# Kernel optimization log

Measured on AMD Instinct MI355X. Metric: run time of the kernel, lower is better.

## Reference

```python
import jax, jax.numpy as jnp
import numpy as np

N_NODES = 100000
N_EDGES = 1600000
IN_CH = 128
HID = 128
BN_EPS = 1e-5


def setup_inputs() -> dict:
    key = jax.random.key(0)
    ks = jax.random.split(key, 16)
    x = jax.random.normal(ks[0], (N_NODES, IN_CH), dtype=jnp.float32)
    edge_index = jax.random.randint(ks[1], (2, N_EDGES), 0, N_NODES, dtype=jnp.int32)
    edge_attr = jax.random.uniform(ks[2], (N_EDGES,), dtype=jnp.float32)
    def glorot(k, fan_in, fan_out):
        s = jnp.sqrt(6.0 / (fan_in + fan_out))
        return jax.random.uniform(k, (fan_in, fan_out), dtype=jnp.float32, minval=-s, maxval=s)
    W1 = glorot(ks[3], IN_CH, HID)
    b1 = jnp.zeros((HID,), jnp.float32)
    gamma1 = jnp.ones((HID,), jnp.float32)
    beta1 = jnp.zeros((HID,), jnp.float32)
    W2 = glorot(ks[4], HID, HID)
    b2 = jnp.zeros((HID,), jnp.float32)
    gamma2 = jnp.ones((HID,), jnp.float32)
    beta2 = jnp.zeros((HID,), jnp.float32)
    W3 = glorot(ks[5], HID, 1)
    b3 = jnp.zeros((1,), jnp.float32)
    return {"x": x, "edge_index": edge_index, "edge_attr": edge_attr,
            "W1": W1, "b1": b1, "gamma1": gamma1, "beta1": beta1,
            "W2": W2, "b2": b2, "gamma2": gamma2, "beta2": beta2,
            "W3": W3, "b3": b3}


def _gcn_norm(edge_index, edge_weight, num_nodes):
    # PyG gcn_norm with add_self_loops=True, self-loop weight 1.0
    sl = jnp.arange(num_nodes, dtype=edge_index.dtype)
    row = jnp.concatenate([edge_index[0], sl])  # source
    col = jnp.concatenate([edge_index[1], sl])  # target
    w = jnp.concatenate([edge_weight, jnp.ones((num_nodes,), edge_weight.dtype)])
    deg = jax.ops.segment_sum(w, col, num_segments=num_nodes)
    dinv = jnp.where(deg > 0, jax.lax.rsqrt(jnp.maximum(deg, 1e-30)), 0.0)
    norm = dinv[row] * w * dinv[col]
    return row, col, norm


def _gcn_conv(x, W, b, row, col, norm, num_nodes):
    xw = x @ W                       # [N, out]
    msg = xw[row] * norm[:, None]    # gather + scale, [E+N, out]
    out = jax.ops.segment_sum(msg, col, num_segments=num_nodes)  # scatter-add
    return out + b


def _batchnorm(x, gamma, beta):
    mean = jnp.mean(x, axis=0)
    var = jnp.mean(jnp.square(x - mean), axis=0)  # biased var (torch BN)
    return (x - mean) * jax.lax.rsqrt(var + BN_EPS) * gamma + beta


def reference(x, edge_index, edge_attr, W1, b1, gamma1, beta1, W2, b2, gamma2, beta2, W3, b3):
    n = x.shape[0]
    row, col, norm = _gcn_norm(edge_index, edge_attr, n)
    h = _gcn_conv(x, W1, b1, row, col, norm, n)
    h = jax.nn.relu(_batchnorm(h, gamma1, beta1))  # dropout = identity (eval)
    h = _gcn_conv(h, W2, b2, row, col, norm, n)
    h = jax.nn.relu(_batchnorm(h, gamma2, beta2))
    out = _gcn_conv(h, W3, b3, row, col, norm, n)  # [N, 1]
    return out
```

## Files before the change

### kernel.cpp

```cpp
#include <hip/hip_runtime.h>
#include <hip/hip_bf16.h>


#define HID 128
#define BN_EPS 1e-5f
#define BK 48
#define NPB 128
#define NBMAX 1024
#define CH_A 6144
#define BINCAP 2432

typedef __attribute__((ext_vector_type(8))) short bf16x8;
typedef __attribute__((ext_vector_type(4))) float f32x4;

static inline size_t alignup(size_t x){ return (x + 255) & ~(size_t)255; }


__global__ __launch_bounds__(256) void k_partA(const int* __restrict__ ei,
    const float* __restrict__ attr, int* __restrict__ binCur,
    int2* __restrict__ binbuf, int E){
  __shared__ int hist[NBMAX];
  __shared__ int pref[NBMAX];
  __shared__ int gbase[NBMAX];
  __shared__ int tmp[256];
  __shared__ int2 stage[CH_A];
  __shared__ unsigned short sbin[CH_A];
  int e0 = blockIdx.x * CH_A;
  for (int b = threadIdx.x; b < NBMAX; b += 256) hist[b] = 0;
  __syncthreads();
  #pragma unroll
  for (int k = 0; k < CH_A/256; ++k){
    int e = e0 + k*256 + threadIdx.x;
    if (e < E) atomicAdd(&hist[ei[E + e] >> 7], 1);
  }
  __syncthreads();
  int b4 = threadIdx.x * 4;
  int h0 = hist[b4], h1 = hist[b4+1], h2 = hist[b4+2], h3 = hist[b4+3];
  int lsum = h0 + h1 + h2 + h3;
  tmp[threadIdx.x] = lsum;
  __syncthreads();
  #pragma unroll
  for (int d = 1; d < 256; d <<= 1){
    int t = (threadIdx.x >= d) ? tmp[threadIdx.x - d] : 0;
    __syncthreads();
    tmp[threadIdx.x] += t;
    __syncthreads();
  }
  int ex = tmp[threadIdx.x] - lsum;
  pref[b4]   = ex;
  pref[b4+1] = ex + h0;
  pref[b4+2] = ex + h0 + h1;
  pref[b4+3] = ex + h0 + h1 + h2;
  gbase[b4]   = h0 ? atomicAdd(&binCur[b4],   h0) : 0;
  gbase[b4+1] = h1 ? atomicAdd(&binCur[b4+1], h1) : 0;
  gbase[b4+2] = h2 ? atomicAdd(&binCur[b4+2], h2) : 0;
  gbase[b4+3] = h3 ? atomicAdd(&binCur[b4+3], h3) : 0;
  hist[b4] = pref[b4]; hist[b4+1] = pref[b4+1];
  hist[b4+2] = pref[b4+2]; hist[b4+3] = pref[b4+3];
  __syncthreads();
  #pragma unroll
  for (int k = 0; k < CH_A/256; ++k){
    int e = e0 + k*256 + threadIdx.x;
    if (e < E){
      int d = ei[E + e];
      int s = ei[e];
      int bin = d >> 7;
      int p = atomicAdd(&hist[bin], 1);
      stage[p] = make_int2(s | ((d & 127) << 17), __float_as_int(attr[e]));
      sbin[p] = (unsigned short)bin;
    }
  }
  __syncthreads();
  int cnt = (e0 + CH_A <= E) ? CH_A : max(E - e0, 0);
  for (int i = threadIdx.x; i < cnt; i += 256){
    int bin = sbin[i];
    int off = gbase[bin] + (i - pref[bin]);
    if (off < BINCAP)
      binbuf[(size_t)bin*BINCAP + off] = stage[i];
  }
}

__global__ __launch_bounds__(256) void k_partB(const int2* __restrict__ binbuf,
    const int* __restrict__ binCur, int2* __restrict__ csr,
    int* __restrict__ cnt, float* __restrict__ degsum, int N){
  __shared__ int2 lb[NPB*BK];
  __shared__ int lcnt[NPB];
  int bin = blockIdx.x;
  int node0 = bin * NPB;
  for (int i = threadIdx.x; i < NPB; i += 256) lcnt[i] = 0;
  __syncthreads();
  int m = min(binCur[bin], BINCAP);
  for (int i = threadIdx.x; i < m; i += 256){
    int2 rec = binbuf[(size_t)bin*BINCAP + i];
    int dlo = (rec.x >> 17) & 127;
    int s   = rec.x & 0x1FFFF;
    int p = atomicAdd(&lcnt[dlo], 1);
    if (p < BK) lb[dlo*BK + p] = make_int2(s, rec.y);
  }
  __syncthreads();
  if (threadIdx.x < NPB){
    int node = node0 + threadIdx.x;
    if (node < N){
      int c = min(lcnt[threadIdx.x], BK);
      float s = 0.f;
      for (int k = 0; k < c; ++k) s += __int_as_float(lb[threadIdx.x*BK + k].y);
      cnt[node] = c;
      degsum[node] = s;
    }
  }
  int lim = min(NPB, N - node0) * BK;
  for (int i = threadIdx.x; i < lim; i += 256)
    csr[(size_t)node0*BK + i] = lb[i];
}

__global__ void k_dinv(const float* __restrict__ degsum, float* __restrict__ dinv, int N){
  int i = blockIdx.x*256 + threadIdx.x;
  if (i < N) dinv[i] = 1.0f / sqrtf(1.0f + degsum[i]);
}

__global__ __launch_bounds__(256) void k_wfin(int2* __restrict__ csr,
    const int* __restrict__ cnt, const float* __restrict__ dinv, int N){
  int node = blockIdx.x*32 + (threadIdx.x >> 3);
  int l = threadIdx.x & 7;
  if (node >= N) return;
  int m = min(cnt[node], BK);
  float di = dinv[node];
  for (int j = l; j < m; j += 8){
    int2 t = csr[(size_t)node*BK + j];
    float w = dinv[t.x] * __int_as_float(t.y) * di;
    csr[(size_t)node*BK + j] = make_int2(t.x, __float_as_int(w));
  }
}


static __device__ inline float2 bf16pair(unsigned int u){
  __hip_bfloat162 h = *(__hip_bfloat162*)&u;
  return __bfloat1622float2(h);
}

static __device__ inline unsigned int packpair(float x, float y){
  __hip_bfloat162 p = __float22bfloat162_rn({x, y});
  return *(unsigned int*)&p;
}

static __device__ inline uint2 pack_bf16x4(float4 a){
  uint2 r;
  r.x = packpair(a.x, a.y);
  r.y = packpair(a.z, a.w);
  return r;
}

static __device__ inline unsigned short bfbits(float v){
  __hip_bfloat16 h = __float2bfloat16(v);
  return *(unsigned short*)&h;
}

__global__ void k_wtprep(const float* __restrict__ Wg, unsigned short* __restrict__ WTg){
  int idx = blockIdx.x*256 + threadIdx.x;
  int k   = idx >> 7;
  int col = idx & 127;
  WTg[(size_t)col*128 + k] = bfbits(Wg[(size_t)k*128 + col]);
}

template<bool BN, bool AB16>
__device__ inline void gemm_body(const void* __restrict__ Av,
    const unsigned short* __restrict__ WTg, const float* __restrict__ coef,
    unsigned int* __restrict__ C, int n, int bid){
  int lane = threadIdx.x & 63;
  int wv4  = threadIdx.x >> 6;
  int l16  = lane & 15;
  int kg   = lane >> 4;
  int row_base = bid*128 + wv4*32;
  int nm1 = n - 1;
  int a0row = min(row_base + l16,      nm1);
  int a1row = min(row_base + 16 + l16, nm1);

  f32x4 acc[2][8] = {};
  #pragma unroll
  for (int k0 = 0; k0 < 128; k0 += 32){
    int k = k0 + kg*8;
    float4 sca, scb, sha, shb;
    if (BN){
      sca = *(const float4*)(coef + k);
      scb = *(const float4*)(coef + k + 4);
      sha = *(const float4*)(coef + 128 + k);
      shb = *(const float4*)(coef + 128 + k + 4);
    }
    bf16x8 a0, a1;
    if constexpr (AB16){
      const unsigned int* A = (const unsigned int*)Av;
      uint4 u0 = *(const uint4*)(A + (size_t)a0row*64 + (k >> 1));
      uint4 u1 = *(const uint4*)(A + (size_t)a1row*64 + (k >> 1));
      #pragma unroll
      for (int half = 0; half < 2; ++half){
        uint4 u = half ? u1 : u0;
        float2 p0 = bf16pair(u.x), p1 = bf16pair(u.y);
        float2 p2 = bf16pair(u.z), p3 = bf16pair(u.w);
        if (BN){
          p0.x = fmaxf(fmaf(p0.x, sca.x, sha.x), 0.f);
          p0.y = fmaxf(fmaf(p0.y, sca.y, sha.y), 0.f);
          p1.x = fmaxf(fmaf(p1.x, sca.z, sha.z), 0.f);
          p1.y = fmaxf(fmaf(p1.y, sca.w, sha.w), 0.f);
          p2.x = fmaxf(fmaf(p2.x, scb.x, shb.x), 0.f);
          p2.y = fmaxf(fmaf(p2.y, scb.y, shb.y), 0.f);
          p3.x = fmaxf(fmaf(p3.x, scb.z, shb.z), 0.f);
          p3.y = fmaxf(fmaf(p3.y, scb.w, shb.w), 0.f);
        }
        union { bf16x8 v; unsigned int u[4]; } c;
        c.u[0] = packpair(p0.x, p0.y);
        c.u[1] = packpair(p1.x, p1.y);
        c.u[2] = packpair(p2.x, p2.y);
        c.u[3] = packpair(p3.x, p3.y);
        if (half) a1 = c.v; else a0 = c.v;
      }
    } else {
      const float* A = (const float*)Av;
      float4 lo0 = *(const float4*)(A + (size_t)a0row*HID + k);
      float4 hi0 = *(const float4*)(A + (size_t)a0row*HID + k + 4);
      float4 lo1 = *(const float4*)(A + (size_t)a1row*HID + k);
      float4 hi1 = *(const float4*)(A + (size_t)a1row*HID + k + 4);
      union { bf16x8 v; uint2 u[2]; } a0c, a1c;
      a0c.u[0] = pack_bf16x4(lo0); a0c.u[1] = pack_bf16x4(hi0);
      a1c.u[0] = pack_bf16x4(lo1); a1c.u[1] = pack_bf16x4(hi1);
      a0 = a0c.v; a1 = a1c.v;
    }
    #pragma unroll
    for (int ct = 0; ct < 8; ++ct){
      int col = ct*16 + l16;
      bf16x8 b = *(const bf16x8*)(WTg + (size_t)col*128 + k);
      acc[0][ct] = __builtin_amdgcn_mfma_f32_16x16x32_bf16(a0, b, acc[0][ct], 0,0,0);
      acc[1][ct] = __builtin_amdgcn_mfma_f32_16x16x32_bf16(a1, b, acc[1][ct], 0,0,0);
    }
  }

  #pragma unroll
  for (int rt = 0; rt < 2; ++rt){
    int growb = row_base + rt*16 + kg*4;
    #pragma unroll
    for (int ct = 0; ct < 8; ++ct){
      #pragma unroll
      for (int r = 0; r < 4; ++r){
        float v = acc[rt][ct][r];
        float o = __shfl_xor(v, 1);
        if (!(lane & 1)){
          int grow = growb + r;
          if (grow < n){
            C[(size_t)grow*64 + ct*8 + (l16 >> 1)] = packpair(v, o);
          }
        }
      }
    }
  }
}

__global__ __launch_bounds__(256) void k_gemm_mfma(const float* __restrict__ A,
    const unsigned short* __restrict__ WTg,
    unsigned int* __restrict__ C, int n){
  gemm_body<false,false>(A, WTg, nullptr, C, n, blockIdx.x);
}

__global__ __launch_bounds__(256) void k_gemm_mfma_bn16(const unsigned int* __restrict__ A,
    const unsigned short* __restrict__ WTg, const float* __restrict__ coef,
    unsigned int* __restrict__ C, int n){
  gemm_body<true,true>(A, WTg, coef, C, n, blockIdx.x);
}


struct Acc8 { float a0,a1,a2,a3,a4,a5,a6,a7; };

static __device__ inline void fma8(Acc8& a, uint4 v, float wt){
  float2 p0 = bf16pair(v.x), p1 = bf16pair(v.y);
  float2 p2 = bf16pair(v.z), p3 = bf16pair(v.w);
  a.a0 = fmaf(wt, p0.x, a.a0); a.a1 = fmaf(wt, p0.y, a.a1);
  a.a2 = fmaf(wt, p1.x, a.a2); a.a3 = fmaf(wt, p1.y, a.a3);
  a.a4 = fmaf(wt, p2.x, a.a4); a.a5 = fmaf(wt, p2.y, a.a5);
  a.a6 = fmaf(wt, p3.x, a.a6); a.a7 = fmaf(wt, p3.y, a.a7);
}

__global__ __launch_bounds__(256) void k_gather128(const unsigned int* __restrict__ xwb,
    const int2* __restrict__ csr, const int* __restrict__ cnt,
    const float* __restrict__ dinv, const float* __restrict__ bias,
    unsigned int* __restrict__ out, int n){
  int node = blockIdx.x*4 + (threadIdx.x >> 6);
  int lane = threadIdx.x & 63;
  if (node >= n) return;
  int l16 = lane & 15;
  int eg  = lane >> 4;
  size_t base = (size_t)node*BK;
  int m = min(cnt[node], BK);
  Acc8 a = {0,0,0,0,0,0,0,0};
  if (eg == 0){
    float di = dinv[node];
    float sw = di * di;
    uint4 sv = *(const uint4*)(xwb + (size_t)node*64 + l16*4);
    float4 b0 = *(const float4*)(bias + l16*8);
    float4 b1 = *(const float4*)(bias + l16*8 + 4);
    a.a0 = b0.x; a.a1 = b0.y; a.a2 = b0.z; a.a3 = b0.w;
    a.a4 = b1.x; a.a5 = b1.y; a.a6 = b1.z; a.a7 = b1.w;
    fma8(a, sv, sw);
  }
  int j = eg;
  for (; j + 12 < m; j += 16){
    int2 e0 = csr[base + j];
    int2 e1 = csr[base + j + 4];
    int2 e2 = csr[base + j + 8];
    int2 e3 = csr[base + j + 12];
    uint4 v0 = *(const uint4*)(xwb + (size_t)e0.x*64 + l16*4);
    uint4 v1 = *(const uint4*)(xwb + (size_t)e1.x*64 + l16*4);
    uint4 v2 = *(const uint4*)(xwb + (size_t)e2.x*64 + l16*4);
    uint4 v3 = *(const uint4*)(xwb + (size_t)e3.x*64 + l16*4);
    fma8(a, v0, __int_as_float(e0.y));
    fma8(a, v1, __int_as_float(e1.y));
    fma8(a, v2, __int_as_float(e2.y));
    fma8(a, v3, __int_as_float(e3.y));
  }
  for (; j < m; j += 4){
    int2 ea = csr[base + j];
    uint4 va = *(const uint4*)(xwb + (size_t)ea.x*64 + l16*4);
    fma8(a, va, __int_as_float(ea.y));
  }
  a.a0 += __shfl_xor(a.a0, 16); a.a1 += __shfl_xor(a.a1, 16);
  a.a2 += __shfl_xor(a.a2, 16); a.a3 += __shfl_xor(a.a3, 16);
  a.a4 += __shfl_xor(a.a4, 16); a.a5 += __shfl_xor(a.a5, 16);
  a.a6 += __shfl_xor(a.a6, 16); a.a7 += __shfl_xor(a.a7, 16);
  a.a0 += __shfl_xor(a.a0, 32); a.a1 += __shfl_xor(a.a1, 32);
  a.a2 += __shfl_xor(a.a2, 32); a.a3 += __shfl_xor(a.a3, 32);
  a.a4 += __shfl_xor(a.a4, 32); a.a5 += __shfl_xor(a.a5, 32);
  a.a6 += __shfl_xor(a.a6, 32); a.a7 += __shfl_xor(a.a7, 32);
  if (eg == 0){
    uint4 r;
    r.x = packpair(a.a0, a.a1);
    r.y = packpair(a.a2, a.a3);
    r.z = packpair(a.a4, a.a5);
    r.w = packpair(a.a6, a.a7);
    *(uint4*)(out + (size_t)node*64 + l16*4) = r;
  }
}

__global__ __launch_bounds__(256) void k_bnstats(const unsigned int* __restrict__ h,
                                                 float* stats, int n){
  __shared__ float ls0[256], ls1[256], lq0[256], lq1[256];
  int p  = threadIdx.x & 63;
  int r0 = blockIdx.x*4 + (threadIdx.x >> 6);
  float s0=0.f, s1=0.f, q0=0.f, q1=0.f;
  for (int r = r0; r < n; r += gridDim.x*4){
    float2 v = bf16pair(h[(size_t)r*64 + p]);
    s0 += v.x; q0 = fmaf(v.x, v.x, q0);
    s1 += v.y; q1 = fmaf(v.y, v.y, q1);
  }
  ls0[threadIdx.x]=s0; ls1[threadIdx.x]=s1; lq0[threadIdx.x]=q0; lq1[threadIdx.x]=q1;
  __syncthreads();
  if (threadIdx.x < 64){
    int t = threadIdx.x;
    s0 = ls0[t]+ls0[t+64]+ls0[t+128]+ls0[t+192];
    s1 = ls1[t]+ls1[t+64]+ls1[t+128]+ls1[t+192];
    q0 = lq0[t]+lq0[t+64]+lq0[t+128]+lq0[t+192];
    q1 = lq1[t]+lq1[t+64]+lq1[t+128]+lq1[t+192];
    atomicAdd(&stats[2*t],       s0);
    atomicAdd(&stats[2*t+1],     s1);
    atomicAdd(&stats[128+2*t],   q0);
    atomicAdd(&stats[128+2*t+1], q1);
  }
}

__global__ void k_bnfin(const float* __restrict__ stats, const float* __restrict__ gamma,
                        const float* __restrict__ beta, float* coef, int n){
  int c = threadIdx.x;
  float inv_n = 1.0f / (float)n;
  float mean = stats[c] * inv_n;
  float var = fmaxf(stats[128 + c] * inv_n - mean*mean, 0.f);
  float sc = gamma[c] / sqrtf(var + BN_EPS);
  coef[c] = sc;
  coef[128 + c] = fmaf(-mean, sc, beta[c]);
}

__global__ __launch_bounds__(256) void k_dotW3(const unsigned int* __restrict__ h,
    const float* __restrict__ coef, const float* __restrict__ W3,
    float* __restrict__ xw3, int n){
  int lane = threadIdx.x & 31;
  int row = blockIdx.x*8 + (threadIdx.x >> 5);
  if (row >= n) return;
  uint2 u = *(const uint2*)(h + (size_t)row*64 + lane*2);
  float2 va = bf16pair(u.x), vb = bf16pair(u.y);
  float4 sc = *(const float4*)(coef + lane*4);
  float4 sh = *(const float4*)(coef + 128 + lane*4);
  float4 w  = *(const float4*)(W3 + lane*4);
  float acc = fmaxf(fmaf(va.x, sc.x, sh.x), 0.f) * w.x
            + fmaxf(fmaf(va.y, sc.y, sh.y), 0.f) * w.y
            + fmaxf(fmaf(vb.x, sc.z, sh.z), 0.f) * w.z
            + fmaxf(fmaf(vb.y, sc.w, sh.w), 0.f) * w.w;
  #pragma unroll
  for (int mm = 1; mm < 32; mm <<= 1) acc += __shfl_xor(acc, mm, 32);
  if (lane == 0) xw3[row] = acc;
}

__global__ void k_gather1(const float* __restrict__ xw3, const int2* __restrict__ csr,
    const int* __restrict__ cnt, const float* __restrict__ dinv,
    const float* __restrict__ b3, float* __restrict__ out, int n){
  int i = blockIdx.x*256 + threadIdx.x;
  if (i >= n) return;
  float di = dinv[i];
  float acc = fmaf(di*di, xw3[i], b3[0]);
  size_t base = (size_t)i*BK;
  int m = min(cnt[i], BK);
  for (int j = 0; j < m; ++j){
    int2 e = csr[base + j];
    acc = fmaf(__int_as_float(e.y), xw3[e.x], acc);
  }
  out[i] = acc;
}

extern "C" void kernel_launch(void* const* d_in, const int* in_sizes, int n_in,
                              void* d_out, int out_size, void* d_ws, size_t ws_size,
                              hipStream_t stream){
  const float* x    = (const float*)d_in[0];
  const int*   ei   = (const int*)  d_in[1];
  const float* attr = (const float*)d_in[2];
  const float* W1   = (const float*)d_in[3];
  const float* b1   = (const float*)d_in[4];
  const float* g1   = (const float*)d_in[5];
  const float* be1  = (const float*)d_in[6];
  const float* W2   = (const float*)d_in[7];
  const float* b2   = (const float*)d_in[8];
  const float* g2   = (const float*)d_in[9];
  const float* be2  = (const float*)d_in[10];
  const float* W3   = (const float*)d_in[11];
  const float* b3   = (const float*)d_in[12];
  float* out = (float*)d_out;

  const int N = in_sizes[0] / HID;
  const int E = in_sizes[2];
  const int nbins = (N + NPB - 1) / NPB;

  char* w = (char*)d_ws;
  auto take = [&](size_t bytes) -> char* { char* p = w; w += alignup(bytes); return p; };
  int*   binCur = (int*)  take((size_t)NBMAX*4);
  int*   cnt    = (int*)  take((size_t)N*4);
  float* degsum = (float*)take((size_t)N*4);
  float* dinv   = (float*)take((size_t)N*4);
  float* stats  = (float*)take(256*4);
  float* coef1  = (float*)take(256*4);
  float* coef2  = (float*)take(256*4);
  unsigned short* wt1 = (unsigned short*)take(128*128*2);
  unsigned short* wt2 = (unsigned short*)take(128*128*2);
  int2*  binbuf = (int2*) take((size_t)nbins*BINCAP*8);
  int2*  csr    = (int2*) take((size_t)N*BK*8);
  float* xw3    = (float*)take((size_t)N*4);
  unsigned int* bufA = (unsigned int*)take((size_t)N*64*4);
  unsigned int* bufB = (unsigned int*)take((size_t)N*64*4);
  (void)ws_size; (void)n_in; (void)out_size;

  int nbN = (N + 255)/256;
  int nbA = (E + CH_A - 1)/CH_A;
  int nbG = (N + 127)/128;
  int nb8 = (N + 31)/32;

  hipMemsetAsync(binCur, 0, (size_t)NBMAX*4, stream);
  k_wtprep   <<<64,    256, 0, stream>>>(W1, wt1);
  k_wtprep   <<<64,    256, 0, stream>>>(W2, wt2);
  k_partA    <<<nbA,   256, 0, stream>>>(ei, attr, binCur, binbuf, E);
  k_gemm_mfma<<<nbG,   256, 0, stream>>>(x, wt1, bufA, N);
  k_partB    <<<nbins, 256, 0, stream>>>(binbuf, binCur, csr, cnt, degsum, N);
  k_dinv     <<<nbN,   256, 0, stream>>>(degsum, dinv, N);
  k_wfin     <<<nb8,   256, 0, stream>>>(csr, cnt, dinv, N);

  k_gather128<<<(N+3)/4, 256, 0, stream>>>(bufA, csr, cnt, dinv, b1, bufB, N);
  hipMemsetAsync(stats, 0, 256*4, stream);
  k_bnstats  <<<512, 256, 0, stream>>>(bufB, stats, N);
  k_bnfin    <<<1, 128, 0, stream>>>(stats, g1, be1, coef1, N);

  k_gemm_mfma_bn16<<<nbG, 256, 0, stream>>>(bufB, wt2, coef1, bufA, N);
  k_gather128<<<(N+3)/4, 256, 0, stream>>>(bufA, csr, cnt, dinv, b2, bufB, N);
  hipMemsetAsync(stats, 0, 256*4, stream);
  k_bnstats  <<<512, 256, 0, stream>>>(bufB, stats, N);
  k_bnfin    <<<1, 128, 0, stream>>>(stats, g2, be2, coef2, N);

  k_dotW3    <<<(N+7)/8, 256, 0, stream>>>(bufB, coef2, W3, xw3, N);
  k_gather1  <<<nbN, 256, 0, stream>>>(xw3, csr, cnt, dinv, b3, out, N);
}
```

Before: 395.9 us.

## Fuse edge partitioning with first GEMM and fold dinv into partB

Runs the edge-binning pass (partA) and the first-layer MFMA GEMM in one launch, with every fourth block doing partitioning and the rest doing GEMM tiles. It also merges the two weight-transpose kernels into one and computes dinv directly in partB, which drops the separate dinv kernel and the degsum buffer. The goal is fewer launches and letting the independent partition and GEMM work overlap on the device. In exchange, every block of the fused kernel reserves the large partition LDS struct, which may lower occupancy for the GEMM blocks.

```diff
diff --git a/kernel.cpp b/kernel.cpp
--- a/kernel.cpp
+++ b/kernel.cpp
@@ -16,47 +16,84 @@
 static inline size_t alignup(size_t x){ return (x + 255) & ~(size_t)255; }
 
 
-__global__ __launch_bounds__(256) void k_partA(const int* __restrict__ ei,
+static __device__ inline float2 bf16pair(unsigned int u){
+  __hip_bfloat162 h = *(__hip_bfloat162*)&u;
+  return __bfloat1622float2(h);
+}
+
+static __device__ inline unsigned int packpair(float x, float y){
+  __hip_bfloat162 p = __float22bfloat162_rn({x, y});
+  return *(unsigned int*)&p;
+}
+
+static __device__ inline uint2 pack_bf16x4(float4 a){
+  uint2 r;
+  r.x = packpair(a.x, a.y);
+  r.y = packpair(a.z, a.w);
+  return r;
+}
+
+static __device__ inline unsigned short bfbits(float v){
+  __hip_bfloat16 h = __float2bfloat16(v);
+  return *(unsigned short*)&h;
+}
+
+__global__ void k_wtprep2(const float* __restrict__ W1, const float* __restrict__ W2,
+                          unsigned short* __restrict__ wt1, unsigned short* __restrict__ wt2){
+  int idx = blockIdx.x*256 + threadIdx.x;
+  const float* Wg = (idx < 16384) ? W1 : W2;
+  unsigned short* WTg = (idx < 16384) ? wt1 : wt2;
+  int i = idx & 16383;
+  int k   = i >> 7;
+  int col = i & 127;
+  WTg[(size_t)col*128 + k] = bfbits(Wg[(size_t)k*128 + col]);
+}
+
+
+struct PartALds {
+  int hist[NBMAX];
+  int pref[NBMAX];
+  int gbase[NBMAX];
+  int tmp[256];
+  int2 stage[CH_A];
+  unsigned short sbin[CH_A];
+};
+
+__device__ inline void partA_body(PartALds& L, const int* __restrict__ ei,
     const float* __restrict__ attr, int* __restrict__ binCur,
-    int2* __restrict__ binbuf, int E){
-  __shared__ int hist[NBMAX];
-  __shared__ int pref[NBMAX];
-  __shared__ int gbase[NBMAX];
-  __shared__ int tmp[256];
-  __shared__ int2 stage[CH_A];
-  __shared__ unsigned short sbin[CH_A];
-  int e0 = blockIdx.x * CH_A;
-  for (int b = threadIdx.x; b < NBMAX; b += 256) hist[b] = 0;
+    int2* __restrict__ binbuf, int E, int aid){
+  int e0 = aid * CH_A;
+  for (int b = threadIdx.x; b < NBMAX; b += 256) L.hist[b] = 0;
   __syncthreads();
   #pragma unroll
   for (int k = 0; k < CH_A/256; ++k){
     int e = e0 + k*256 + threadIdx.x;
-    if (e < E) atomicAdd(&hist[ei[E + e] >> 7], 1);
+    if (e < E) atomicAdd(&L.hist[ei[E + e] >> 7], 1);
   }
   __syncthreads();
   int b4 = threadIdx.x * 4;
-  int h0 = hist[b4], h1 = hist[b4+1], h2 = hist[b4+2], h3 = hist[b4+3];
+  int h0 = L.hist[b4], h1 = L.hist[b4+1], h2 = L.hist[b4+2], h3 = L.hist[b4+3];
   int lsum = h0 + h1 + h2 + h3;
-  tmp[threadIdx.x] = lsum;
+  L.tmp[threadIdx.x] = lsum;
   __syncthreads();
   #pragma unroll
   for (int d = 1; d < 256; d <<= 1){
-    int t = (threadIdx.x >= d) ? tmp[threadIdx.x - d] : 0;
+    int t = (threadIdx.x >= d) ? L.tmp[threadIdx.x - d] : 0;
     __syncthreads();
-    tmp[threadIdx.x] += t;
+    L.tmp[threadIdx.x] += t;
     __syncthreads();
   }
-  int ex = tmp[threadIdx.x] - lsum;
-  pref[b4]   = ex;
-  pref[b4+1] = ex + h0;
-  pref[b4+2] = ex + h0 + h1;
-  pref[b4+3] = ex + h0 + h1 + h2;
-  gbase[b4]   = h0 ? atomicAdd(&binCur[b4],   h0) : 0;
-  gbase[b4+1] = h1 ? atomicAdd(&binCur[b4+1], h1) : 0;
-  gbase[b4+2] = h2 ? atomicAdd(&binCur[b4+2], h2) : 0;
-  gbase[b4+3] = h3 ? atomicAdd(&binCur[b4+3], h3) : 0;
-  hist[b4] = pref[b4]; hist[b4+1] = pref[b4+1];
-  hist[b4+2] = pref[b4+2]; hist[b4+3] = pref[b4+3];
+  int ex = L.tmp[threadIdx.x] - lsum;
+  L.pref[b4]   = ex;
+  L.pref[b4+1] = ex + h0;
+  L.pref[b4+2] = ex + h0 + h1;
+  L.pref[b4+3] = ex + h0 + h1 + h2;
+  L.gbase[b4]   = h0 ? atomicAdd(&binCur[b4],   h0) : 0;
+  L.gbase[b4+1] = h1 ? atomicAdd(&binCur[b4+1], h1) : 0;
+  L.gbase[b4+2] = h2 ? atomicAdd(&binCur[b4+2], h2) : 0;
+  L.gbase[b4+3] = h3 ? atomicAdd(&binCur[b4+3], h3) : 0;
+  L.hist[b4] = L.pref[b4]; L.hist[b4+1] = L.pref[b4+1];
+  L.hist[b4+2] = L.pref[b4+2]; L.hist[b4+3] = L.pref[b4+3];
   __syncthreads();
   #pragma unroll
   for (int k = 0; k < CH_A/256; ++k){
@@ -65,102 +102,21 @@
       int d = ei[E + e];
       int s = ei[e];
       int bin = d >> 7;
-      int p = atomicAdd(&hist[bin], 1);
-      stage[p] = make_int2(s | ((d & 127) << 17), __float_as_int(attr[e]));
-      sbin[p] = (unsigned short)bin;
+      int p = atomicAdd(&L.hist[bin], 1);
+      L.stage[p] = make_int2(s | ((d & 127) << 17), __float_as_int(attr[e]));
+      L.sbin[p] = (unsigned short)bin;
     }
   }
   __syncthreads();
   int cnt = (e0 + CH_A <= E) ? CH_A : max(E - e0, 0);
   for (int i = threadIdx.x; i < cnt; i += 256){
-    int bin = sbin[i];
-    int off = gbase[bin] + (i - pref[bin]);
+    int bin = L.sbin[i];
+    int off = L.gbase[bin] + (i - L.pref[bin]);
     if (off < BINCAP)
-      binbuf[(size_t)bin*BINCAP + off] = stage[i];
-  }
-}
-
-__global__ __launch_bounds__(256) void k_partB(const int2* __restrict__ binbuf,
-    const int* __restrict__ binCur, int2* __restrict__ csr,
-    int* __restrict__ cnt, float* __restrict__ degsum, int N){
-  __shared__ int2 lb[NPB*BK];
-  __shared__ int lcnt[NPB];
-  int bin = blockIdx.x;
-  int node0 = bin * NPB;
-  for (int i = threadIdx.x; i < NPB; i += 256) lcnt[i] = 0;
-  __syncthreads();
-  int m = min(binCur[bin], BINCAP);
-  for (int i = threadIdx.x; i < m; i += 256){
-    int2 rec = binbuf[(size_t)bin*BINCAP + i];
-    int dlo = (rec.x >> 17) & 127;
-    int s   = rec.x & 0x1FFFF;
-    int p = atomicAdd(&lcnt[dlo], 1);
-    if (p < BK) lb[dlo*BK + p] = make_int2(s, rec.y);
-  }
-  __syncthreads();
-  if (threadIdx.x < NPB){
-    int node = node0 + threadIdx.x;
-    if (node < N){
-      int c = min(lcnt[threadIdx.x], BK);
-      float s = 0.f;
-      for (int k = 0; k < c; ++k) s += __int_as_float(lb[threadIdx.x*BK + k].y);
-      cnt[node] = c;
-      degsum[node] = s;
-    }
-  }
-  int lim = min(NPB, N - node0) * BK;
-  for (int i = threadIdx.x; i < lim; i += 256)
-    csr[(size_t)node0*BK + i] = lb[i];
-}
-
-__global__ void k_dinv(const float* __restrict__ degsum, float* __restrict__ dinv, int N){
-  int i = blockIdx.x*256 + threadIdx.x;
-  if (i < N) dinv[i] = 1.0f / sqrtf(1.0f + degsum[i]);
-}
-
-__global__ __launch_bounds__(256) void k_wfin(int2* __restrict__ csr,
-    const int* __restrict__ cnt, const float* __restrict__ dinv, int N){
-  int node = blockIdx.x*32 + (threadIdx.x >> 3);
-  int l = threadIdx.x & 7;
-  if (node >= N) return;
-  int m = min(cnt[node], BK);
-  float di = dinv[node];
-  for (int j = l; j < m; j += 8){
-    int2 t = csr[(size_t)node*BK + j];
-    float w = dinv[t.x] * __int_as_float(t.y) * di;
-    csr[(size_t)node*BK + j] = make_int2(t.x, __float_as_int(w));
-  }
-}
-
-
-static __device__ inline float2 bf16pair(unsigned int u){
-  __hip_bfloat162 h = *(__hip_bfloat162*)&u;
-  return __bfloat1622float2(h);
-}
-
-static __device__ inline unsigned int packpair(float x, float y){
-  __hip_bfloat162 p = __float22bfloat162_rn({x, y});
-  return *(unsigned int*)&p;
-}
-
-static __device__ inline uint2 pack_bf16x4(float4 a){
-  uint2 r;
-  r.x = packpair(a.x, a.y);
-  r.y = packpair(a.z, a.w);
-  return r;
-}
-
-static __device__ inline unsigned short bfbits(float v){
-  __hip_bfloat16 h = __float2bfloat16(v);
-  return *(unsigned short*)&h;
-}
-
-__global__ void k_wtprep(const float* __restrict__ Wg, unsigned short* __restrict__ WTg){
-  int idx = blockIdx.x*256 + threadIdx.x;
-  int k   = idx >> 7;
-  int col = idx & 127;
-  WTg[(size_t)col*128 + k] = bfbits(Wg[(size_t)k*128 + col]);
-}
+      binbuf[(size_t)bin*BINCAP + off] = L.stage[i];
+  }
+}
+
 
 template<bool BN, bool AB16>
 __device__ inline void gemm_body(const void* __restrict__ Av,
@@ -253,16 +209,74 @@
   }
 }
 
-__global__ __launch_bounds__(256) void k_gemm_mfma(const float* __restrict__ A,
-    const unsigned short* __restrict__ WTg,
+__global__ __launch_bounds__(256) void k_partA_gemm(
+    const int* __restrict__ ei, const float* __restrict__ attr,
+    int* __restrict__ binCur, int2* __restrict__ binbuf, int E, int nbA,
+    const float* __restrict__ A, const unsigned short* __restrict__ WTg,
     unsigned int* __restrict__ C, int n){
-  gemm_body<false,false>(A, WTg, nullptr, C, n, blockIdx.x);
+  __shared__ PartALds L;
+  int bid = blockIdx.x;
+  int q = bid >> 2, r = bid & 3;
+  if (r == 0 && q < nbA){
+    partA_body(L, ei, attr, binCur, binbuf, E, q);
+  } else {
+    int aBefore = min(q + (r ? 1 : 0), nbA);
+    gemm_body<false,false>(A, WTg, nullptr, C, n, bid - aBefore);
+  }
 }
 
 __global__ __launch_bounds__(256) void k_gemm_mfma_bn16(const unsigned int* __restrict__ A,
     const unsigned short* __restrict__ WTg, const float* __restrict__ coef,
     unsigned int* __restrict__ C, int n){
   gemm_body<true,true>(A, WTg, coef, C, n, blockIdx.x);
+}
+
+
+__global__ __launch_bounds__(256) void k_partB(const int2* __restrict__ binbuf,
+    const int* __restrict__ binCur, int2* __restrict__ csr,
+    int* __restrict__ cnt, float* __restrict__ dinv, int N){
+  __shared__ int2 lb[NPB*BK];
+  __shared__ int lcnt[NPB];
+  int bin = blockIdx.x;
+  int node0 = bin * NPB;
+  for (int i = threadIdx.x; i < NPB; i += 256) lcnt[i] = 0;
+  __syncthreads();
+  int m = min(binCur[bin], BINCAP);
+  for (int i = threadIdx.x; i < m; i += 256){
+    int2 rec = binbuf[(size_t)bin*BINCAP + i];
+    int dlo = (rec.x >> 17) & 127;
+    int s   = rec.x & 0x1FFFF;
+    int p = atomicAdd(&lcnt[dlo], 1);
+    if (p < BK) lb[dlo*BK + p] = make_int2(s, rec.y);
+  }
+  __syncthreads();
+  if (threadIdx.x < NPB){
+    int node = node0 + threadIdx.x;
+    if (node < N){
+      int c = min(lcnt[threadIdx.x], BK);
+      float s = 0.f;
+      for (int k = 0; k < c; ++k) s += __int_as_float(lb[threadIdx.x*BK + k].y);
+      cnt[node] = c;
+      dinv[node] = 1.0f / sqrtf(1.0f + s);
+    }
+  }
+  int lim = min(NPB, N - node0) * BK;
+  for (int i = threadIdx.x; i < lim; i += 256)
+    csr[(size_t)node0*BK + i] = lb[i];
+}
+
+__global__ __launch_bounds__(256) void k_wfin(int2* __restrict__ csr,
+    const int* __restrict__ cnt, const float* __restrict__ dinv, int N){
+  int node = blockIdx.x*32 + (threadIdx.x >> 3);
+  int l = threadIdx.x & 7;
+  if (node >= N) return;
+  int m = min(cnt[node], BK);
+  float di = dinv[node];
+  for (int j = l; j < m; j += 8){
+    int2 t = csr[(size_t)node*BK + j];
+    float w = dinv[t.x] * __int_as_float(t.y) * di;
+    csr[(size_t)node*BK + j] = make_int2(t.x, __float_as_int(w));
+  }
 }
 
 
@@ -436,7 +450,6 @@
   auto take = [&](size_t bytes) -> char* { char* p = w; w += alignup(bytes); return p; };
   int*   binCur = (int*)  take((size_t)NBMAX*4);
   int*   cnt    = (int*)  take((size_t)N*4);
-  float* degsum = (float*)take((size_t)N*4);
   float* dinv   = (float*)take((size_t)N*4);
   float* stats  = (float*)take(256*4);
   float* coef1  = (float*)take(256*4);
@@ -456,13 +469,11 @@
   int nb8 = (N + 31)/32;
 
   hipMemsetAsync(binCur, 0, (size_t)NBMAX*4, stream);
-  k_wtprep   <<<64,    256, 0, stream>>>(W1, wt1);
-  k_wtprep   <<<64,    256, 0, stream>>>(W2, wt2);
-  k_partA    <<<nbA,   256, 0, stream>>>(ei, attr, binCur, binbuf, E);
-  k_gemm_mfma<<<nbG,   256, 0, stream>>>(x, wt1, bufA, N);
-  k_partB    <<<nbins, 256, 0, stream>>>(binbuf, binCur, csr, cnt, degsum, N);
-  k_dinv     <<<nbN,   256, 0, stream>>>(degsum, dinv, N);
-  k_wfin     <<<nb8,   256, 0, stream>>>(csr, cnt, dinv, N);
+  k_wtprep2   <<<128,       256, 0, stream>>>(W1, W2, wt1, wt2);
+  k_partA_gemm<<<nbA + nbG, 256, 0, stream>>>(ei, attr, binCur, binbuf, E, nbA,
+                                              x, wt1, bufA, N);
+  k_partB     <<<nbins,     256, 0, stream>>>(binbuf, binCur, csr, cnt, dinv, N);
+  k_wfin      <<<nb8,       256, 0, stream>>>(csr, cnt, dinv, N);
 
   k_gather128<<<(N+3)/4, 256, 0, stream>>>(bufA, csr, cnt, dinv, b1, bufB, N);
   hipMemsetAsync(stats, 0, 256*4, stream);
```

Result: slower. 406.6 us (+2.7%).

## Factor symmetric GCN normalization into source pre-scale and destination post-scale

Applied to the files above, without the earlier changes.

The symmetric normalization dinv[src]*w*dinv[dst] is split so each GEMM epilogue scales its output rows by dinv, and each gather applies dinv[dst] plus bias at the end. This removes the k_wfin pass that rewrote every CSR edge weight, and the separate k_dinv kernel, since dinv is now computed inside partB. It also merges the two weight-prep launches into one. Storing pre-scaled bf16 values shifts where rounding happens, and GEMM1 must now wait for partB instead of running alongside it.

```diff
diff --git a/kernel.cpp b/kernel.cpp
--- a/kernel.cpp
+++ b/kernel.cpp
@@ -14,6 +14,40 @@
 typedef __attribute__((ext_vector_type(4))) float f32x4;
 
 static inline size_t alignup(size_t x){ return (x + 255) & ~(size_t)255; }
+
+
+static __device__ inline float2 bf16pair(unsigned int u){
+  __hip_bfloat162 h = *(__hip_bfloat162*)&u;
+  return __bfloat1622float2(h);
+}
+
+static __device__ inline unsigned int packpair(float x, float y){
+  __hip_bfloat162 p = __float22bfloat162_rn({x, y});
+  return *(unsigned int*)&p;
+}
+
+static __device__ inline uint2 pack_bf16x4(float4 a){
+  uint2 r;
+  r.x = packpair(a.x, a.y);
+  r.y = packpair(a.z, a.w);
+  return r;
+}
+
+static __device__ inline unsigned short bfbits(float v){
+  __hip_bfloat16 h = __float2bfloat16(v);
+  return *(unsigned short*)&h;
+}
+
+__global__ void k_wtprep2(const float* __restrict__ W1, const float* __restrict__ W2,
+                          unsigned short* __restrict__ wt1, unsigned short* __restrict__ wt2){
+  int idx = blockIdx.x*256 + threadIdx.x;
+  const float* Wg = (idx < 16384) ? W1 : W2;
+  unsigned short* WTg = (idx < 16384) ? wt1 : wt2;
+  int i = idx & 16383;
+  int k   = i >> 7;
+  int col = i & 127;
+  WTg[(size_t)col*128 + k] = bfbits(Wg[(size_t)k*128 + col]);
+}
 
 
 __global__ __launch_bounds__(256) void k_partA(const int* __restrict__ ei,
@@ -82,7 +116,7 @@
 
 __global__ __launch_bounds__(256) void k_partB(const int2* __restrict__ binbuf,
     const int* __restrict__ binCur, int2* __restrict__ csr,
-    int* __restrict__ cnt, float* __restrict__ degsum, int N){
+    int* __restrict__ cnt, float* __restrict__ dinv, int N){
   __shared__ int2 lb[NPB*BK];
   __shared__ int lcnt[NPB];
   int bin = blockIdx.x;
@@ -105,7 +139,7 @@
       float s = 0.f;
       for (int k = 0; k < c; ++k) s += __int_as_float(lb[threadIdx.x*BK + k].y);
       cnt[node] = c;
-      degsum[node] = s;
+      dinv[node] = 1.0f / sqrtf(1.0f + s);
     }
   }
   int lim = min(NPB, N - node0) * BK;
@@ -113,58 +147,10 @@
     csr[(size_t)node0*BK + i] = lb[i];
 }
 
-__global__ void k_dinv(const float* __restrict__ degsum, float* __restrict__ dinv, int N){
-  int i = blockIdx.x*256 + threadIdx.x;
-  if (i < N) dinv[i] = 1.0f / sqrtf(1.0f + degsum[i]);
-}
-
-__global__ __launch_bounds__(256) void k_wfin(int2* __restrict__ csr,
-    const int* __restrict__ cnt, const float* __restrict__ dinv, int N){
-  int node = blockIdx.x*32 + (threadIdx.x >> 3);
-  int l = threadIdx.x & 7;
-  if (node >= N) return;
-  int m = min(cnt[node], BK);
-  float di = dinv[node];
-  for (int j = l; j < m; j += 8){
-    int2 t = csr[(size_t)node*BK + j];
-    float w = dinv[t.x] * __int_as_float(t.y) * di;
-    csr[(size_t)node*BK + j] = make_int2(t.x, __float_as_int(w));
-  }
-}
-
-
-static __device__ inline float2 bf16pair(unsigned int u){
-  __hip_bfloat162 h = *(__hip_bfloat162*)&u;
-  return __bfloat1622float2(h);
-}
-
-static __device__ inline unsigned int packpair(float x, float y){
-  __hip_bfloat162 p = __float22bfloat162_rn({x, y});
-  return *(unsigned int*)&p;
-}
-
-static __device__ inline uint2 pack_bf16x4(float4 a){
-  uint2 r;
-  r.x = packpair(a.x, a.y);
-  r.y = packpair(a.z, a.w);
-  return r;
-}
-
-static __device__ inline unsigned short bfbits(float v){
-  __hip_bfloat16 h = __float2bfloat16(v);
-  return *(unsigned short*)&h;
-}
-
-__global__ void k_wtprep(const float* __restrict__ Wg, unsigned short* __restrict__ WTg){
-  int idx = blockIdx.x*256 + threadIdx.x;
-  int k   = idx >> 7;
-  int col = idx & 127;
-  WTg[(size_t)col*128 + k] = bfbits(Wg[(size_t)k*128 + col]);
-}
-
 template<bool BN, bool AB16>
 __device__ inline void gemm_body(const void* __restrict__ Av,
     const unsigned short* __restrict__ WTg, const float* __restrict__ coef,
+    const float* __restrict__ dinv,
     unsigned int* __restrict__ C, int n, int bid){
   int lane = threadIdx.x & 63;
   int wv4  = threadIdx.x >> 6;
@@ -237,32 +223,31 @@
   for (int rt = 0; rt < 2; ++rt){
     int growb = row_base + rt*16 + kg*4;
     #pragma unroll
-    for (int ct = 0; ct < 8; ++ct){
+    for (int r = 0; r < 4; ++r){
+      int grow = growb + r;
+      bool ok = (grow < n) && !(lane & 1);
+      float dv = ok ? dinv[grow] : 0.f;
       #pragma unroll
-      for (int r = 0; r < 4; ++r){
+      for (int ct = 0; ct < 8; ++ct){
         float v = acc[rt][ct][r];
         float o = __shfl_xor(v, 1);
-        if (!(lane & 1)){
-          int grow = growb + r;
-          if (grow < n){
-            C[(size_t)grow*64 + ct*8 + (l16 >> 1)] = packpair(v, o);
-          }
-        }
+        if (ok)
+          C[(size_t)grow*64 + ct*8 + (l16 >> 1)] = packpair(v*dv, o*dv);
       }
     }
   }
 }
 
-__global__ __launch_bounds__(256) void k_gemm_mfma(const float* __restrict__ A,
-    const unsigned short* __restrict__ WTg,
+__global__ __launch_bounds__(256) void k_gemm_mfma_s(const float* __restrict__ A,
+    const unsigned short* __restrict__ WTg, const float* __restrict__ dinv,
     unsigned int* __restrict__ C, int n){
-  gemm_body<false,false>(A, WTg, nullptr, C, n, blockIdx.x);
-}
-
-__global__ __launch_bounds__(256) void k_gemm_mfma_bn16(const unsigned int* __restrict__ A,
+  gemm_body<false,false>(A, WTg, nullptr, dinv, C, n, blockIdx.x);
+}
+
+__global__ __launch_bounds__(256) void k_gemm_mfma_bn16_s(const unsigned int* __restrict__ A,
     const unsigned short* __restrict__ WTg, const float* __restrict__ coef,
-    unsigned int* __restrict__ C, int n){
-  gemm_body<true,true>(A, WTg, coef, C, n, blockIdx.x);
+    const float* __restrict__ dinv, unsigned int* __restrict__ C, int n){
+  gemm_body<true,true>(A, WTg, coef, dinv, C, n, blockIdx.x);
 }
 
 
@@ -277,7 +262,7 @@
   a.a6 = fmaf(wt, p3.x, a.a6); a.a7 = fmaf(wt, p3.y, a.a7);
 }
 
-__global__ __launch_bounds__(256) void k_gather128(const unsigned int* __restrict__ xwb,
+__global__ __launch_bounds__(256) void k_gather128(const unsigned int* __restrict__ yb,
     const int2* __restrict__ csr, const int* __restrict__ cnt,
     const float* __restrict__ dinv, const float* __restrict__ bias,
     unsigned int* __restrict__ out, int n){
@@ -289,15 +274,17 @@
   size_t base = (size_t)node*BK;
   int m = min(cnt[node], BK);
   Acc8 a = {0,0,0,0,0,0,0,0};
+  float di = 0.f;
+  float4 b0 = {0,0,0,0}, b1 = {0,0,0,0};
   if (eg == 0){
-    float di = dinv[node];
-    float sw = di * di;
-    uint4 sv = *(const uint4*)(xwb + (size_t)node*64 + l16*4);
-    float4 b0 = *(const float4*)(bias + l16*8);
-    float4 b1 = *(const float4*)(bias + l16*8 + 4);
-    a.a0 = b0.x; a.a1 = b0.y; a.a2 = b0.z; a.a3 = b0.w;
-    a.a4 = b1.x; a.a5 = b1.y; a.a6 = b1.z; a.a7 = b1.w;
-    fma8(a, sv, sw);
+    di = dinv[node];
+    uint4 sv = *(const uint4*)(yb + (size_t)node*64 + l16*4);
+    b0 = *(const float4*)(bias + l16*8);
+    b1 = *(const float4*)(bias + l16*8 + 4);
+    float2 p0 = bf16pair(sv.x), p1 = bf16pair(sv.y);
+    float2 p2 = bf16pair(sv.z), p3 = bf16pair(sv.w);
+    a.a0 = p0.x; a.a1 = p0.y; a.a2 = p1.x; a.a3 = p1.y;
+    a.a4 = p2.x; a.a5 = p2.y; a.a6 = p3.x; a.a7 = p3.y;
   }
   int j = eg;
   for (; j + 12 < m; j += 16){
@@ -305,10 +292,10 @@
     int2 e1 = csr[base + j + 4];
     int2 e2 = csr[base + j + 8];
     int2 e3 = csr[base + j + 12];
-    uint4 v0 = *(const uint4*)(xwb + (size_t)e0.x*64 + l16*4);
-    uint4 v1 = *(const uint4*)(xwb + (size_t)e1.x*64 + l16*4);
-    uint4 v2 = *(const uint4*)(xwb + (size_t)e2.x*64 + l16*4);
-    uint4 v3 = *(const uint4*)(xwb + (size_t)e3.x*64 + l16*4);
+    uint4 v0 = *(const uint4*)(yb + (size_t)e0.x*64 + l16*4);
+    uint4 v1 = *(const uint4*)(yb + (size_t)e1.x*64 + l16*4);
+    uint4 v2 = *(const uint4*)(yb + (size_t)e2.x*64 + l16*4);
+    uint4 v3 = *(const uint4*)(yb + (size_t)e3.x*64 + l16*4);
     fma8(a, v0, __int_as_float(e0.y));
     fma8(a, v1, __int_as_float(e1.y));
     fma8(a, v2, __int_as_float(e2.y));
@@ -316,7 +303,7 @@
   }
   for (; j < m; j += 4){
     int2 ea = csr[base + j];
-    uint4 va = *(const uint4*)(xwb + (size_t)ea.x*64 + l16*4);
+    uint4 va = *(const uint4*)(yb + (size_t)ea.x*64 + l16*4);
     fma8(a, va, __int_as_float(ea.y));
   }
   a.a0 += __shfl_xor(a.a0, 16); a.a1 += __shfl_xor(a.a1, 16);
@@ -329,10 +316,10 @@
   a.a6 += __shfl_xor(a.a6, 32); a.a7 += __shfl_xor(a.a7, 32);
   if (eg == 0){
     uint4 r;
-    r.x = packpair(a.a0, a.a1);
-    r.y = packpair(a.a2, a.a3);
-    r.z = packpair(a.a4, a.a5);
-    r.w = packpair(a.a6, a.a7);
+    r.x = packpair(fmaf(di, a.a0, b0.x), fmaf(di, a.a1, b0.y));
+    r.y = packpair(fmaf(di, a.a2, b0.z), fmaf(di, a.a3, b0.w));
+    r.z = packpair(fmaf(di, a.a4, b1.x), fmaf(di, a.a5, b1.y));
+    r.w = packpair(fmaf(di, a.a6, b1.z), fmaf(di, a.a7, b1.w));
     *(uint4*)(out + (size_t)node*64 + l16*4) = r;
   }
 }
@@ -376,7 +363,7 @@
 
 __global__ __launch_bounds__(256) void k_dotW3(const unsigned int* __restrict__ h,
     const float* __restrict__ coef, const float* __restrict__ W3,
-    float* __restrict__ xw3, int n){
+    const float* __restrict__ dinv, float* __restrict__ y3, int n){
   int lane = threadIdx.x & 31;
   int row = blockIdx.x*8 + (threadIdx.x >> 5);
   if (row >= n) return;
@@ -391,23 +378,22 @@
             + fmaxf(fmaf(vb.y, sc.w, sh.w), 0.f) * w.w;
   #pragma unroll
   for (int mm = 1; mm < 32; mm <<= 1) acc += __shfl_xor(acc, mm, 32);
-  if (lane == 0) xw3[row] = acc;
-}
-
-__global__ void k_gather1(const float* __restrict__ xw3, const int2* __restrict__ csr,
+  if (lane == 0) y3[row] = acc * dinv[row];
+}
+
+__global__ void k_gather1(const float* __restrict__ y3, const int2* __restrict__ csr,
     const int* __restrict__ cnt, const float* __restrict__ dinv,
     const float* __restrict__ b3, float* __restrict__ out, int n){
   int i = blockIdx.x*256 + threadIdx.x;
   if (i >= n) return;
-  float di = dinv[i];
-  float acc = fmaf(di*di, xw3[i], b3[0]);
+  float acc = y3[i];
   size_t base = (size_t)i*BK;
   int m = min(cnt[i], BK);
   for (int j = 0; j < m; ++j){
     int2 e = csr[base + j];
-    acc = fmaf(__int_as_float(e.y), xw3[e.x], acc);
-  }
-  out[i] = acc;
+    acc = fmaf(__int_as_float(e.y), y3[e.x], acc);
+  }
+  out[i] = fmaf(dinv[i], acc, b3[0]);
 }
 
 extern "C" void kernel_launch(void* const* d_in, const int* in_sizes, int n_in,
@@ -436,7 +422,6 @@
   auto take = [&](size_t bytes) -> char* { char* p = w; w += alignup(bytes); return p; };
   int*   binCur = (int*)  take((size_t)NBMAX*4);
   int*   cnt    = (int*)  take((size_t)N*4);
-  float* degsum = (float*)take((size_t)N*4);
   float* dinv   = (float*)take((size_t)N*4);
   float* stats  = (float*)take(256*4);
   float* coef1  = (float*)take(256*4);
@@ -445,7 +430,7 @@
   unsigned short* wt2 = (unsigned short*)take(128*128*2);
   int2*  binbuf = (int2*) take((size_t)nbins*BINCAP*8);
   int2*  csr    = (int2*) take((size_t)N*BK*8);
-  float* xw3    = (float*)take((size_t)N*4);
+  float* y3     = (float*)take((size_t)N*4);
   unsigned int* bufA = (unsigned int*)take((size_t)N*64*4);
   unsigned int* bufB = (unsigned int*)take((size_t)N*64*4);
   (void)ws_size; (void)n_in; (void)out_size;
@@ -453,28 +438,24 @@
   int nbN = (N + 255)/256;
   int nbA = (E + CH_A - 1)/CH_A;
   int nbG = (N + 127)/128;
-  int nb8 = (N + 31)/32;
 
   hipMemsetAsync(binCur, 0, (size_t)NBMAX*4, stream);
-  k_wtprep   <<<64,    256, 0, stream>>>(W1, wt1);
-  k_wtprep   <<<64,    256, 0, stream>>>(W2, wt2);
+  k_wtprep2  <<<128,   256, 0, stream>>>(W1, W2, wt1, wt2);
   k_partA    <<<nbA,   256, 0, stream>>>(ei, attr, binCur, binbuf, E);
-  k_gemm_mfma<<<nbG,   256, 0, stream>>>(x, wt1, bufA, N);
-  k_partB    <<<nbins, 256, 0, stream>>>(binbuf, binCur, csr, cnt, degsum, N);
-  k_dinv     <<<nbN,   256, 0, stream>>>(degsum, dinv, N);
-  k_wfin     <<<nb8,   256, 0, stream>>>(csr, cnt, dinv, N);
+  k_partB    <<<nbins, 256, 0, stream>>>(binbuf, binCur, csr, cnt, dinv, N);
+  k_gemm_mfma_s<<<nbG, 256, 0, stream>>>(x, wt1, dinv, bufA, N);
 
   k_gather128<<<(N+3)/4, 256, 0, stream>>>(bufA, csr, cnt, dinv, b1, bufB, N);
   hipMemsetAsync(stats, 0, 256*4, stream);
   k_bnstats  <<<512, 256, 0, stream>>>(bufB, stats, N);
   k_bnfin    <<<1, 128, 0, stream>>>(stats, g1, be1, coef1, N);
 
-  k_gemm_mfma_bn16<<<nbG, 256, 0, stream>>>(bufB, wt2, coef1, bufA, N);
+  k_gemm_mfma_bn16_s<<<nbG, 256, 0, stream>>>(bufB, wt2, coef1, dinv, bufA, N);
   k_gather128<<<(N+3)/4, 256, 0, stream>>>(bufA, csr, cnt, dinv, b2, bufB, N);
   hipMemsetAsync(stats, 0, 256*4, stream);
   k_bnstats  <<<512, 256, 0, stream>>>(bufB, stats, N);
   k_bnfin    <<<1, 128, 0, stream>>>(stats, g2, be2, coef2, N);
 
-  k_dotW3    <<<(N+7)/8, 256, 0, stream>>>(bufB, coef2, W3, xw3, N);
-  k_gather1  <<<nbN, 256, 0, stream>>>(xw3, csr, cnt, dinv, b3, out, N);
-}
+  k_dotW3    <<<(N+7)/8, 256, 0, stream>>>(bufB, coef2, W3, dinv, y3, N);
+  k_gather1  <<<nbN, 256, 0, stream>>>(y3, csr, cnt, dinv, b3, out, N);
+}
```

Result: no change. 399.5 us (+0.9%).
